# Kernel optimization log

Hardware: AMD Instinct MI355X
Metric: run time of the kernel (lower is better)

## Reference

```python
import jax, jax.numpy as jnp
import numpy as np

N_HEAD = 16
HEAD_DIM = 64  # n_embd // n_head = 1024 // 16


def setup_inputs() -> dict:
    key = jax.random.key(0)
    k1, k2, k3 = jax.random.split(key, 3)
    B, S, D = 2, 2048, 1024
    x = jax.random.normal(k1, (B, S, D), dtype=jnp.float32)
    # torch nn.Linear stores weight [out, in]; we keep [in, out] for x @ W
    w_qkv = jax.random.normal(k2, (D, 3 * D), dtype=jnp.float32) * (D ** -0.5)
    w_proj = jax.random.normal(k3, (D, D), dtype=jnp.float32) * (D ** -0.5)
    return {"x": x, "w_qkv": w_qkv, "w_proj": w_proj}


def reference(x, w_qkv, w_proj):
    B, S, D = x.shape
    qkv = x @ w_qkv  # [B, S, 3D]
    q, k, v = jnp.split(qkv, 3, axis=-1)
    # [B, H, S, hd]
    q = q.reshape(B, S, N_HEAD, HEAD_DIM).transpose(0, 2, 1, 3)
    k = k.reshape(B, S, N_HEAD, HEAD_DIM).transpose(0, 2, 1, 3)
    v = v.reshape(B, S, N_HEAD, HEAD_DIM).transpose(0, 2, 1, 3)
    att = jnp.einsum('bhid,bhjd->bhij', q, k) * (HEAD_DIM ** -0.5)
    causal = jnp.tril(jnp.ones((S, S), dtype=bool))
    att = jnp.where(causal, att, jnp.finfo(att.dtype).min)
    att = jax.nn.softmax(att, axis=-1)
    # dropout p=0 (eval) -> identity
    y = jnp.einsum('bhij,bhjd->bhid', att, v)
    y = y.transpose(0, 2, 1, 3).reshape(B, S, D)
    return y @ w_proj
```

## Files before the change

kernel.cpp:

```cpp
#include <hip/hip_runtime.h>

#define AS1 __attribute__((address_space(1)))
#define AS3 __attribute__((address_space(3)))

using f32x4 = __attribute__((ext_vector_type(4))) float;
using s16x8 = __attribute__((ext_vector_type(8))) short;
using u16x4 = __attribute__((ext_vector_type(4))) unsigned short;
using u32x2 = __attribute__((ext_vector_type(2))) unsigned int;

__device__ __forceinline__ unsigned short f2bf(float f) {
  union { float f; unsigned u; } v; v.f = f;
  unsigned u = v.u;
  return (unsigned short)((u + 0x7FFFu + ((u >> 16) & 1u)) >> 16);
}

__device__ __forceinline__ unsigned pack_bf2(float a, float b) {
  union { float f; unsigned u; } x, y; x.f = a; y.f = b;
  return (x.u >> 16) | (y.u & 0xFFFF0000u);
}

__device__ __forceinline__ void load_lds16(const void* g, void* l) {
  __builtin_amdgcn_global_load_lds((const AS1 void*)g, (AS3 void*)l, 16, 0, 0);
}

__global__ __launch_bounds__(256) void prep_kernel(const float* __restrict__ x,
                                                   const float* __restrict__ w_qkv,
                                                   const float* __restrict__ w_proj,
                                                   unsigned short* __restrict__ xb,
                                                   unsigned short* __restrict__ wqkvT,
                                                   unsigned short* __restrict__ wprojT) {
  __shared__ float tile[32][33];
  const int bid = blockIdx.x, tid = threadIdx.x;
  if (bid < 4096) {
    int i = bid * 256 + tid;
    float4 v = ((const float4*)x)[i];
    u16x4 o;
    o.x = f2bf(v.x); o.y = f2bf(v.y); o.z = f2bf(v.z); o.w = f2bf(v.w);
    ((u16x4*)xb)[i] = o;
    return;
  }
  const float* in;
  unsigned short* out;
  int bx, by, R, C;
  if (bid < 7168) {
    int t = bid - 4096;
    bx = t % 96; by = t / 96; R = 1024; C = 3072;
    in = w_qkv; out = wqkvT;
  } else {
    int t = bid - 7168;
    bx = t % 32; by = t / 32; R = 1024; C = 1024;
    in = w_proj; out = wprojT;
  }
  const int tx = tid & 31, ty = tid >> 5;
  int xcol = bx * 32 + tx;
  int y0 = by * 32;
  for (int j = ty; j < 32; j += 8)
    tile[j][tx] = in[(size_t)(y0 + j) * C + xcol];
  __syncthreads();
  int x2 = by * 32 + tx;
  int y2 = bx * 32;
  for (int j = ty; j < 32; j += 8)
    out[(size_t)(y2 + j) * R + x2] = f2bf(tile[tx][j]);
}

__global__ __launch_bounds__(256) void transpose_v(const unsigned short* __restrict__ qkv,
                                                   unsigned short* __restrict__ Vt) {
  __shared__ unsigned short tile[64][65];
  const int tid = threadIdx.x;
  const int bh = blockIdx.y, b = bh >> 4, h = bh & 15;
  const int s0 = blockIdx.x * 64;
#pragma unroll
  for (int it = 0; it < 2; ++it) {
    int c = tid + it * 256;
    int row = c >> 3, cc = c & 7;
    s16x8 v = *(const s16x8*)(qkv + (size_t)(b * 2048 + s0 + row) * 3072 + 2048 + h * 64 + cc * 8);
#pragma unroll
    for (int j = 0; j < 8; ++j) tile[row][cc * 8 + j] = (unsigned short)v[j];
  }
  __syncthreads();
#pragma unroll
  for (int it = 0; it < 2; ++it) {
    int c = tid + it * 256;
    int d = c >> 3, sc = c & 7;
    s16x8 o;
#pragma unroll
    for (int j = 0; j < 8; ++j) o[j] = (short)tile[sc * 8 + j][d];
    *(s16x8*)(Vt + (size_t)bh * 64 * 2048 + (size_t)d * 2048 + s0 + sc * 8) = o;
  }
}

__global__ __launch_bounds__(256) void gemm_qkv(const unsigned short* __restrict__ A,
                                                const unsigned short* __restrict__ Bt,
                                                unsigned short* __restrict__ C,
                                                int M, int N, int K) {
  __shared__ unsigned short As[128 * 64];
  __shared__ unsigned short Bs[128 * 64];
  const int tid = threadIdx.x;
  const int wave = tid >> 6, lane = tid & 63;
  const int l15 = lane & 15, quad = lane >> 4;
  const int sx = l15 & 7;
  const int wm = wave & 1, wn = wave >> 1;
  const int bm = blockIdx.y, bn = blockIdx.x;

  f32x4 acc[4][4] = {};

  for (int k0 = 0; k0 < K; k0 += 64) {
    __syncthreads();
#pragma unroll
    for (int s = 0; s < 4; ++s) {
      int c = tid + s * 256;
      int row = c >> 3, cc = c & 7;
      int kc = (cc ^ (row & 7)) * 8;
      load_lds16(A + (size_t)(bm * 128 + row) * K + k0 + kc, As + c * 8);
      load_lds16(Bt + (size_t)(bn * 128 + row) * K + k0 + kc, Bs + c * 8);
    }
    __syncthreads();
#pragma unroll
    for (int kk = 0; kk < 2; ++kk) {
      s16x8 af[4], bfr[4];
#pragma unroll
      for (int i = 0; i < 4; ++i) {
        af[i]  = *(const s16x8*)(As + (wm * 64 + i * 16 + l15) * 64 + ((quad + 4 * kk) ^ sx) * 8);
        bfr[i] = *(const s16x8*)(Bs + (wn * 64 + i * 16 + l15) * 64 + ((quad + 4 * kk) ^ sx) * 8);
      }
#pragma unroll
      for (int i = 0; i < 4; ++i)
#pragma unroll
        for (int j = 0; j < 4; ++j)
          acc[i][j] = __builtin_amdgcn_mfma_f32_16x16x32_bf16(af[i], bfr[j], acc[i][j], 0, 0, 0);
    }
  }

  const int row0 = bm * 128 + wm * 64 + quad * 4;
  const int col0 = bn * 128 + wn * 64 + l15;
#pragma unroll
  for (int i = 0; i < 4; ++i)
#pragma unroll
    for (int j = 0; j < 4; ++j)
#pragma unroll
      for (int r = 0; r < 4; ++r)
        C[(size_t)(row0 + i * 16 + r) * N + (col0 + j * 16)] = f2bf(acc[i][j][r]);
}

__global__ __launch_bounds__(256) void gemm_proj(const unsigned short* __restrict__ A,
                                                 const unsigned short* __restrict__ Bt,
                                                 float* __restrict__ C,
                                                 int M, int N, int K) {
  __shared__ unsigned short As[128 * 64];
  __shared__ unsigned short Bs[64 * 64];
  const int tid = threadIdx.x;
  const int wave = tid >> 6, lane = tid & 63;
  const int l15 = lane & 15, quad = lane >> 4;
  const int sx = l15 & 7;
  const int wm = wave & 1, wn = wave >> 1;
  const int bm = blockIdx.y, bn = blockIdx.x;

  f32x4 acc[4][2] = {};

  for (int k0 = 0; k0 < K; k0 += 64) {
    __syncthreads();
#pragma unroll
    for (int s = 0; s < 4; ++s) {
      int c = tid + s * 256;
      int row = c >> 3, cc = c & 7;
      int kc = (cc ^ (row & 7)) * 8;
      load_lds16(A + (size_t)(bm * 128 + row) * K + k0 + kc, As + c * 8);
    }
#pragma unroll
    for (int s = 0; s < 2; ++s) {
      int c = tid + s * 256;
      int row = c >> 3, cc = c & 7;
      int kc = (cc ^ (row & 7)) * 8;
      load_lds16(Bt + (size_t)(bn * 64 + row) * K + k0 + kc, Bs + c * 8);
    }
    __syncthreads();
#pragma unroll
    for (int kk = 0; kk < 2; ++kk) {
      s16x8 af[4], bfr[2];
#pragma unroll
      for (int i = 0; i < 4; ++i)
        af[i] = *(const s16x8*)(As + (wm * 64 + i * 16 + l15) * 64 + ((quad + 4 * kk) ^ sx) * 8);
#pragma unroll
      for (int j = 0; j < 2; ++j)
        bfr[j] = *(const s16x8*)(Bs + (wn * 32 + j * 16 + l15) * 64 + ((quad + 4 * kk) ^ sx) * 8);
#pragma unroll
      for (int i = 0; i < 4; ++i)
#pragma unroll
        for (int j = 0; j < 2; ++j)
          acc[i][j] = __builtin_amdgcn_mfma_f32_16x16x32_bf16(af[i], bfr[j], acc[i][j], 0, 0, 0);
    }
  }

  const int row0 = bm * 128 + wm * 64 + quad * 4;
  const int col0 = bn * 64 + wn * 32 + l15;
#pragma unroll
  for (int i = 0; i < 4; ++i)
#pragma unroll
    for (int j = 0; j < 2; ++j)
#pragma unroll
      for (int r = 0; r < 4; ++r)
        C[(size_t)(row0 + i * 16 + r) * N + (col0 + j * 16)] = acc[i][j][r];
}

__global__ __launch_bounds__(512) void attn_kernel(const unsigned short* __restrict__ qkv,
                                                   const unsigned short* __restrict__ Vt,
                                                   unsigned short* __restrict__ Y) {
  __shared__ unsigned short Qs[128 * 64];
  __shared__ unsigned short Ks[64 * 64];
  __shared__ unsigned short Vs[64 * 64];
  const int tid = threadIdx.x;
  const int wave = tid >> 6, lane = tid & 63;
  const int l15 = lane & 15, quad = lane >> 4;
  const int sx = l15 & 7, sx2 = sx << 1;

  const int p = blockIdx.x;
  const int r_ = p >> 8, c_ = p & 255;
  const int m_ = c_ & 15, g_ = c_ >> 4;
  const int bh = g_ + 16 * r_;
  const int lq = r_ ? (15 - m_) : m_;
  const int q0 = lq * 128;
  const int b = bh >> 4, h = bh & 15;
  const size_t base = (size_t)b * 2048 * 3072 + h * 64;
  const size_t vbase = (size_t)bh * 64 * 2048;

#pragma unroll
  for (int s = 0; s < 2; ++s) {
    int cid = tid + s * 512;
    int row = cid >> 3, cc = cid & 7;
    int kc = (cc ^ (row & 7)) * 8;
    load_lds16(qkv + base + (size_t)(q0 + row) * 3072 + kc, Qs + cid * 8);
  }
  __syncthreads();
  s16x8 qf[2];
  qf[0] = *(const s16x8*)(Qs + (wave * 16 + l15) * 64 + ((quad    ) ^ sx) * 8);
  qf[1] = *(const s16x8*)(Qs + (wave * 16 + l15) * 64 + ((quad + 4) ^ sx) * 8);

  f32x4 o[4] = {};
  float m_i = -1e30f, l_i = 0.f;
  const float kScale = 0.125f * 1.44269504f;
  const int qrow_w0 = q0 + wave * 16;
  const int qrow = qrow_w0 + l15;
  unsigned short* Pw = Qs + wave * 16 * 64;

  for (int j0 = 0; j0 <= q0 + 64; j0 += 64) {
    __syncthreads();
    {
      int row = tid >> 3, cc = tid & 7;
      int kc = (cc ^ (row & 7)) * 8;
      load_lds16(qkv + base + (size_t)(j0 + row) * 3072 + 1024 + kc, Ks + tid * 8);
      load_lds16(Vt + vbase + (size_t)row * 2048 + j0 + kc, Vs + tid * 8);
    }
    __syncthreads();

    if (j0 <= qrow_w0 + 15) {
      f32x4 s[4];
#pragma unroll
      for (int nt = 0; nt < 4; ++nt) {
        const int kr = nt * 16 + l15;
        s16x8 kf0 = *(const s16x8*)(Ks + kr * 64 + ((quad    ) ^ sx) * 8);
        s16x8 kf1 = *(const s16x8*)(Ks + kr * 64 + ((quad + 4) ^ sx) * 8);
        f32x4 z = {};
        z = __builtin_amdgcn_mfma_f32_16x16x32_bf16(kf0, qf[0], z, 0, 0, 0);
        z = __builtin_amdgcn_mfma_f32_16x16x32_bf16(kf1, qf[1], z, 0, 0, 0);
        s[nt] = z;
      }

      if (j0 + 63 > qrow_w0) {
#pragma unroll
        for (int nt = 0; nt < 4; ++nt) {
          int key0 = j0 + nt * 16 + quad * 4;
#pragma unroll
          for (int r = 0; r < 4; ++r)
            if (key0 + r > qrow) s[nt][r] = -3e38f;
        }
      }

      float tmax = s[0][0];
#pragma unroll
      for (int nt = 0; nt < 4; ++nt)
#pragma unroll
        for (int r = 0; r < 4; ++r)
          tmax = fmaxf(tmax, s[nt][r]);
      tmax = fmaxf(tmax, __shfl_xor(tmax, 16, 64));
      tmax = fmaxf(tmax, __shfl_xor(tmax, 32, 64));
      float mn = fmaxf(m_i, tmax);
      float alpha = __builtin_amdgcn_exp2f((m_i - mn) * kScale);
      m_i = mn;
      const float mk = mn * kScale;
      float rsum = 0.f;
#pragma unroll
      for (int nt = 0; nt < 4; ++nt)
#pragma unroll
        for (int r = 0; r < 4; ++r) {
          float pv = __builtin_amdgcn_exp2f(__builtin_fmaf(s[nt][r], kScale, -mk));
          s[nt][r] = pv;
          rsum += pv;
        }
      rsum += __shfl_xor(rsum, 16, 64);
      rsum += __shfl_xor(rsum, 32, 64);
      l_i = l_i * alpha + rsum;
#pragma unroll
      for (int dt = 0; dt < 4; ++dt)
#pragma unroll
        for (int r = 0; r < 4; ++r)
          o[dt][r] *= alpha;

#pragma unroll
      for (int nt = 0; nt < 4; ++nt) {
        u32x2 pk;
        pk.x = pack_bf2(s[nt][0], s[nt][1]);
        pk.y = pack_bf2(s[nt][2], s[nt][3]);
        int phys = (nt * 4 + quad) ^ sx2;
        *(u32x2*)(Pw + l15 * 64 + phys * 4) = pk;
      }

      s16x8 pf[2];
      pf[0] = *(const s16x8*)(Pw + l15 * 64 + (((quad * 2)    ) ^ sx2) * 4);
      pf[1] = *(const s16x8*)(Pw + l15 * 64 + (((quad * 2) + 8) ^ sx2) * 4);

#pragma unroll
      for (int dt = 0; dt < 4; ++dt) {
        const int vr = dt * 16 + l15;
        s16x8 vf0 = *(const s16x8*)(Vs + vr * 64 + ((quad    ) ^ sx) * 8);
        s16x8 vf1 = *(const s16x8*)(Vs + vr * 64 + ((quad + 4) ^ sx) * 8);
        o[dt] = __builtin_amdgcn_mfma_f32_16x16x32_bf16(vf0, pf[0], o[dt], 0, 0, 0);
        o[dt] = __builtin_amdgcn_mfma_f32_16x16x32_bf16(vf1, pf[1], o[dt], 0, 0, 0);
      }
    }
  }

  const float inv = 1.0f / l_i;
  const size_t yoff = (size_t)(b * 2048 + qrow) * 1024 + h * 64 + quad * 4;
#pragma unroll
  for (int dt = 0; dt < 4; ++dt) {
    u16x4 pk;
#pragma unroll
    for (int r = 0; r < 4; ++r) pk[r] = f2bf(o[dt][r] * inv);
    *(u16x4*)(Y + yoff + dt * 16) = pk;
  }
}

extern "C" void kernel_launch(void* const* d_in, const int* in_sizes, int n_in,
                              void* d_out, int out_size, void* d_ws, size_t ws_size,
                              hipStream_t stream) {
  const float* x      = (const float*)d_in[0];
  const float* w_qkv  = (const float*)d_in[1];
  const float* w_proj = (const float*)d_in[2];
  char* ws = (char*)d_ws;
  unsigned short* xb     = (unsigned short*)(ws);
  unsigned short* wqkvT  = (unsigned short*)(ws + (size_t)(8  << 20));
  unsigned short* wprojT = (unsigned short*)(ws + (size_t)(14 << 20));
  unsigned short* qkv    = (unsigned short*)(ws + (size_t)(16 << 20));
  unsigned short* y      = (unsigned short*)(ws + (size_t)(40 << 20));
  unsigned short* Vt     = (unsigned short*)(ws + (size_t)(48 << 20));

  prep_kernel<<<8192, 256, 0, stream>>>(x, w_qkv, w_proj, xb, wqkvT, wprojT);
  gemm_qkv<<<dim3(24, 32), 256, 0, stream>>>(xb, wqkvT, qkv, 4096, 3072, 1024);
  transpose_v<<<dim3(32, 32), 256, 0, stream>>>(qkv, Vt);
  attn_kernel<<<512, 512, 0, stream>>>(qkv, Vt, y);
  gemm_proj<<<dim3(16, 32), 256, 0, stream>>>(y, wprojT, (float*)d_out, 4096, 1024, 1024);
}
```

Measured before the change: 182.9 us.

## Split long causal attention rows across blocks with LUT schedule and combine pass

Attention tiles shrink from 128 to 64 query rows with 256-thread blocks. A constant lookup table gives each of 1536 blocks a query tile and key range. The longer query tiles (t>=16) are split into two key halves whose partial outputs, maxes and sums go to fp32 workspace, and a new combine kernel merges them. The aim is to balance causal work across CUs and shorten the critical path. The cost is an extra kernel launch and partial-result traffic.

New measurement: 188.3 us. 2.9% more time.

```diff
diff --git a/kernel.cpp b/kernel.cpp
--- a/kernel.cpp
+++ b/kernel.cpp
@@ -22,6 +22,16 @@
 __device__ __forceinline__ void load_lds16(const void* g, void* l) {
   __builtin_amdgcn_global_load_lds((const AS1 void*)g, (AS3 void*)l, 16, 0, 0);
 }
+
+__constant__ unsigned char LUT_T[48] = {
+  15,30,31, 8, 7, 0,   31,14,13, 9,16, 1,   28,29,12,10,17, 2,   29,26,24,11,16, 3,
+  30,27,25,22, 6, 4,   27,25,23,20,18, 5,   28,23,21,19,19,17,   26,24,21,22,20,18};
+__constant__ unsigned char LUT_JB[48] = {
+   0, 0, 0, 0, 0, 0,   16, 0, 0, 0, 0, 0,    0, 0, 0, 0, 0, 0,   15, 0, 0, 0, 9, 0,
+  16, 0, 0, 0, 0, 0,   14,13, 0, 0, 0, 0,   15,12, 0, 0,10, 9,   14,13,11,12,11,10};
+__constant__ unsigned char LUT_JE[48] = {
+  16,16,16, 9, 8, 1,   32,15,14,10, 9, 2,   15,15,13,11, 9, 3,   30,14,13,12,17, 4,
+  31,14,13,12, 7, 5,   28,26,12,11,10, 6,   29,24,11,10,20,18,   27,25,22,23,21,19};
 
 __global__ __launch_bounds__(256) void prep_kernel(const float* __restrict__ x,
                                                    const float* __restrict__ w_qkv,
@@ -202,10 +212,13 @@
         C[(size_t)(row0 + i * 16 + r) * N + (col0 + j * 16)] = acc[i][j][r];
 }
 
-__global__ __launch_bounds__(512) void attn_kernel(const unsigned short* __restrict__ qkv,
+__global__ __launch_bounds__(256) void attn_kernel(const unsigned short* __restrict__ qkv,
                                                    const unsigned short* __restrict__ Vt,
-                                                   unsigned short* __restrict__ Y) {
-  __shared__ unsigned short Qs[128 * 64];
+                                                   unsigned short* __restrict__ Y,
+                                                   float* __restrict__ PO,
+                                                   float* __restrict__ PM,
+                                                   float* __restrict__ PL) {
+  __shared__ unsigned short Qs[64 * 64];
   __shared__ unsigned short Ks[64 * 64];
   __shared__ unsigned short Vs[64 * 64];
   const int tid = threadIdx.x;
@@ -214,18 +227,18 @@
   const int sx = l15 & 7, sx2 = sx << 1;
 
   const int p = blockIdx.x;
-  const int r_ = p >> 8, c_ = p & 255;
-  const int m_ = c_ & 15, g_ = c_ >> 4;
-  const int bh = g_ + 16 * r_;
-  const int lq = r_ ? (15 - m_) : m_;
-  const int q0 = lq * 128;
+  const int c_ = p & 255, a_ = p >> 8;
+  const int col = c_ & 7, bh = c_ >> 3;
+  const int li = col * 6 + a_;
+  const int t = LUT_T[li], jbeg = LUT_JB[li], jend = LUT_JE[li];
+  const int q0 = t * 64;
   const int b = bh >> 4, h = bh & 15;
   const size_t base = (size_t)b * 2048 * 3072 + h * 64;
   const size_t vbase = (size_t)bh * 64 * 2048;
 
 #pragma unroll
   for (int s = 0; s < 2; ++s) {
-    int cid = tid + s * 512;
+    int cid = tid + s * 256;
     int row = cid >> 3, cc = cid & 7;
     int kc = (cc ^ (row & 7)) * 8;
     load_lds16(qkv + base + (size_t)(q0 + row) * 3072 + kc, Qs + cid * 8);
@@ -242,101 +255,139 @@
   const int qrow = qrow_w0 + l15;
   unsigned short* Pw = Qs + wave * 16 * 64;
 
-  for (int j0 = 0; j0 <= q0 + 64; j0 += 64) {
-    __syncthreads();
-    {
-      int row = tid >> 3, cc = tid & 7;
+  for (int jt = jbeg; jt < jend; ++jt) {
+    const int j0 = jt * 64;
+    __syncthreads();
+#pragma unroll
+    for (int s = 0; s < 2; ++s) {
+      int c = tid + s * 256;
+      int row = c >> 3, cc = c & 7;
       int kc = (cc ^ (row & 7)) * 8;
-      load_lds16(qkv + base + (size_t)(j0 + row) * 3072 + 1024 + kc, Ks + tid * 8);
-      load_lds16(Vt + vbase + (size_t)row * 2048 + j0 + kc, Vs + tid * 8);
-    }
-    __syncthreads();
-
-    if (j0 <= qrow_w0 + 15) {
-      f32x4 s[4];
+      load_lds16(qkv + base + (size_t)(j0 + row) * 3072 + 1024 + kc, Ks + c * 8);
+      load_lds16(Vt + vbase + (size_t)row * 2048 + j0 + kc, Vs + c * 8);
+    }
+    __syncthreads();
+
+    f32x4 s[4];
+#pragma unroll
+    for (int nt = 0; nt < 4; ++nt) {
+      const int kr = nt * 16 + l15;
+      s16x8 kf0 = *(const s16x8*)(Ks + kr * 64 + ((quad    ) ^ sx) * 8);
+      s16x8 kf1 = *(const s16x8*)(Ks + kr * 64 + ((quad + 4) ^ sx) * 8);
+      f32x4 z = {};
+      z = __builtin_amdgcn_mfma_f32_16x16x32_bf16(kf0, qf[0], z, 0, 0, 0);
+      z = __builtin_amdgcn_mfma_f32_16x16x32_bf16(kf1, qf[1], z, 0, 0, 0);
+      s[nt] = z;
+    }
+
+    if (j0 + 63 > qrow_w0) {
 #pragma unroll
       for (int nt = 0; nt < 4; ++nt) {
-        const int kr = nt * 16 + l15;
-        s16x8 kf0 = *(const s16x8*)(Ks + kr * 64 + ((quad    ) ^ sx) * 8);
-        s16x8 kf1 = *(const s16x8*)(Ks + kr * 64 + ((quad + 4) ^ sx) * 8);
-        f32x4 z = {};
-        z = __builtin_amdgcn_mfma_f32_16x16x32_bf16(kf0, qf[0], z, 0, 0, 0);
-        z = __builtin_amdgcn_mfma_f32_16x16x32_bf16(kf1, qf[1], z, 0, 0, 0);
-        s[nt] = z;
+        int key0 = j0 + nt * 16 + quad * 4;
+#pragma unroll
+        for (int r = 0; r < 4; ++r)
+          if (key0 + r > qrow) s[nt][r] = -3e38f;
       }
-
-      if (j0 + 63 > qrow_w0) {
-#pragma unroll
-        for (int nt = 0; nt < 4; ++nt) {
-          int key0 = j0 + nt * 16 + quad * 4;
-#pragma unroll
-          for (int r = 0; r < 4; ++r)
-            if (key0 + r > qrow) s[nt][r] = -3e38f;
-        }
+    }
+
+    float tmax = s[0][0];
+#pragma unroll
+    for (int nt = 0; nt < 4; ++nt)
+#pragma unroll
+      for (int r = 0; r < 4; ++r)
+        tmax = fmaxf(tmax, s[nt][r]);
+    tmax = fmaxf(tmax, __shfl_xor(tmax, 16, 64));
+    tmax = fmaxf(tmax, __shfl_xor(tmax, 32, 64));
+    float mn = fmaxf(m_i, tmax);
+    float alpha = __builtin_amdgcn_exp2f((m_i - mn) * kScale);
+    m_i = mn;
+    const float mk = mn * kScale;
+    float rsum = 0.f;
+#pragma unroll
+    for (int nt = 0; nt < 4; ++nt)
+#pragma unroll
+      for (int r = 0; r < 4; ++r) {
+        float pv = __builtin_amdgcn_exp2f(__builtin_fmaf(s[nt][r], kScale, -mk));
+        s[nt][r] = pv;
+        rsum += pv;
       }
-
-      float tmax = s[0][0];
-#pragma unroll
-      for (int nt = 0; nt < 4; ++nt)
-#pragma unroll
-        for (int r = 0; r < 4; ++r)
-          tmax = fmaxf(tmax, s[nt][r]);
-      tmax = fmaxf(tmax, __shfl_xor(tmax, 16, 64));
-      tmax = fmaxf(tmax, __shfl_xor(tmax, 32, 64));
-      float mn = fmaxf(m_i, tmax);
-      float alpha = __builtin_amdgcn_exp2f((m_i - mn) * kScale);
-      m_i = mn;
-      const float mk = mn * kScale;
-      float rsum = 0.f;
-#pragma unroll
-      for (int nt = 0; nt < 4; ++nt)
-#pragma unroll
-        for (int r = 0; r < 4; ++r) {
-          float pv = __builtin_amdgcn_exp2f(__builtin_fmaf(s[nt][r], kScale, -mk));
-          s[nt][r] = pv;
-          rsum += pv;
-        }
-      rsum += __shfl_xor(rsum, 16, 64);
-      rsum += __shfl_xor(rsum, 32, 64);
-      l_i = l_i * alpha + rsum;
-#pragma unroll
-      for (int dt = 0; dt < 4; ++dt)
-#pragma unroll
-        for (int r = 0; r < 4; ++r)
-          o[dt][r] *= alpha;
-
-#pragma unroll
-      for (int nt = 0; nt < 4; ++nt) {
-        u32x2 pk;
-        pk.x = pack_bf2(s[nt][0], s[nt][1]);
-        pk.y = pack_bf2(s[nt][2], s[nt][3]);
-        int phys = (nt * 4 + quad) ^ sx2;
-        *(u32x2*)(Pw + l15 * 64 + phys * 4) = pk;
-      }
-
-      s16x8 pf[2];
-      pf[0] = *(const s16x8*)(Pw + l15 * 64 + (((quad * 2)    ) ^ sx2) * 4);
-      pf[1] = *(const s16x8*)(Pw + l15 * 64 + (((quad * 2) + 8) ^ sx2) * 4);
-
-#pragma unroll
-      for (int dt = 0; dt < 4; ++dt) {
-        const int vr = dt * 16 + l15;
-        s16x8 vf0 = *(const s16x8*)(Vs + vr * 64 + ((quad    ) ^ sx) * 8);
-        s16x8 vf1 = *(const s16x8*)(Vs + vr * 64 + ((quad + 4) ^ sx) * 8);
-        o[dt] = __builtin_amdgcn_mfma_f32_16x16x32_bf16(vf0, pf[0], o[dt], 0, 0, 0);
-        o[dt] = __builtin_amdgcn_mfma_f32_16x16x32_bf16(vf1, pf[1], o[dt], 0, 0, 0);
-      }
-    }
-  }
-
-  const float inv = 1.0f / l_i;
-  const size_t yoff = (size_t)(b * 2048 + qrow) * 1024 + h * 64 + quad * 4;
-#pragma unroll
-  for (int dt = 0; dt < 4; ++dt) {
-    u16x4 pk;
-#pragma unroll
-    for (int r = 0; r < 4; ++r) pk[r] = f2bf(o[dt][r] * inv);
-    *(u16x4*)(Y + yoff + dt * 16) = pk;
+    rsum += __shfl_xor(rsum, 16, 64);
+    rsum += __shfl_xor(rsum, 32, 64);
+    l_i = l_i * alpha + rsum;
+#pragma unroll
+    for (int dt = 0; dt < 4; ++dt)
+#pragma unroll
+      for (int r = 0; r < 4; ++r)
+        o[dt][r] *= alpha;
+
+#pragma unroll
+    for (int nt = 0; nt < 4; ++nt) {
+      u32x2 pk;
+      pk.x = pack_bf2(s[nt][0], s[nt][1]);
+      pk.y = pack_bf2(s[nt][2], s[nt][3]);
+      int phys = (nt * 4 + quad) ^ sx2;
+      *(u32x2*)(Pw + l15 * 64 + phys * 4) = pk;
+    }
+
+    s16x8 pf[2];
+    pf[0] = *(const s16x8*)(Pw + l15 * 64 + (((quad * 2)    ) ^ sx2) * 4);
+    pf[1] = *(const s16x8*)(Pw + l15 * 64 + (((quad * 2) + 8) ^ sx2) * 4);
+
+#pragma unroll
+    for (int dt = 0; dt < 4; ++dt) {
+      const int vr = dt * 16 + l15;
+      s16x8 vf0 = *(const s16x8*)(Vs + vr * 64 + ((quad    ) ^ sx) * 8);
+      s16x8 vf1 = *(const s16x8*)(Vs + vr * 64 + ((quad + 4) ^ sx) * 8);
+      o[dt] = __builtin_amdgcn_mfma_f32_16x16x32_bf16(vf0, pf[0], o[dt], 0, 0, 0);
+      o[dt] = __builtin_amdgcn_mfma_f32_16x16x32_bf16(vf1, pf[1], o[dt], 0, 0, 0);
+    }
+  }
+
+  if (t < 16) {
+    const float inv = 1.0f / l_i;
+    const size_t yoff = (size_t)(b * 2048 + qrow) * 1024 + h * 64 + quad * 4;
+#pragma unroll
+    for (int dt = 0; dt < 4; ++dt) {
+      u16x4 pk;
+#pragma unroll
+      for (int r = 0; r < 4; ++r) pk[r] = f2bf(o[dt][r] * inv);
+      *(u16x4*)(Y + yoff + dt * 16) = pk;
+    }
+  } else {
+    const int half = (jbeg == 0) ? 0 : 1;
+    const int idx = (bh * 16 + (t - 16)) * 2 + half;
+    const int qlocal = wave * 16 + l15;
+    float* POb = PO + (size_t)idx * 4096 + qlocal * 64;
+#pragma unroll
+    for (int dt = 0; dt < 4; ++dt)
+      *(f32x4*)(POb + dt * 16 + quad * 4) = o[dt];
+    if (quad == 0) {
+      PM[idx * 64 + qlocal] = m_i;
+      PL[idx * 64 + qlocal] = l_i;
+    }
+  }
+}
+
+__global__ __launch_bounds__(256) void attn_combine(const float* __restrict__ PO,
+                                                    const float* __restrict__ PM,
+                                                    const float* __restrict__ PL,
+                                                    unsigned short* __restrict__ Y) {
+  const int tid = threadIdx.x;
+  const int d = tid & 63;
+  const float kScale = 0.125f * 1.44269504f;
+  for (int it = 0; it < 16; ++it) {
+    int R = blockIdx.x * 64 + it * 4 + (tid >> 6);
+    int bh = R >> 10, rem = R & 1023, tp = rem >> 6, q = rem & 63;
+    int i2 = (bh * 16 + tp) * 2;
+    float m1 = PM[i2 * 64 + q], l1 = PL[i2 * 64 + q];
+    float m2 = PM[(i2 + 1) * 64 + q], l2 = PL[(i2 + 1) * 64 + q];
+    float m = fmaxf(m1, m2);
+    float a1 = __builtin_amdgcn_exp2f((m1 - m) * kScale);
+    float a2 = __builtin_amdgcn_exp2f((m2 - m) * kScale);
+    size_t o1 = (size_t)i2 * 4096 + q * 64 + d;
+    float v = (PO[o1] * a1 + PO[o1 + 4096] * a2) / (l1 * a1 + l2 * a2);
+    int b = bh >> 4, h = bh & 15, qrow = (tp + 16) * 64 + q;
+    Y[(size_t)(b * 2048 + qrow) * 1024 + h * 64 + d] = f2bf(v);
   }
 }
 
@@ -353,10 +404,14 @@
   unsigned short* qkv    = (unsigned short*)(ws + (size_t)(16 << 20));
   unsigned short* y      = (unsigned short*)(ws + (size_t)(40 << 20));
   unsigned short* Vt     = (unsigned short*)(ws + (size_t)(48 << 20));
+  float*          PO     = (float*)(ws + (size_t)(56 << 20));
+  float*          PM     = (float*)(ws + (size_t)(73 << 20));
+  float*          PL     = (float*)(ws + (size_t)(74 << 20));
 
   prep_kernel<<<8192, 256, 0, stream>>>(x, w_qkv, w_proj, xb, wqkvT, wprojT);
   gemm_qkv<<<dim3(24, 32), 256, 0, stream>>>(xb, wqkvT, qkv, 4096, 3072, 1024);
   transpose_v<<<dim3(32, 32), 256, 0, stream>>>(qkv, Vt);
-  attn_kernel<<<512, 512, 0, stream>>>(qkv, Vt, y);
+  attn_kernel<<<1536, 256, 0, stream>>>(qkv, Vt, y, PO, PM, PL);
+  attn_combine<<<512, 256, 0, stream>>>(PO, PM, PL, y);
   gemm_proj<<<dim3(16, 32), 256, 0, stream>>>(y, wprojT, (float*)d_out, 4096, 1024, 1024);
 }
```

## Compute V transposed directly via GEMM and double-buffer K/V tiles in attention

Applied to the files above, without the earlier changes.

Splits the QKV projection into a Q/K GEMM and a separate GEMM that writes V already transposed (W_v^T · x^T), so the standalone V transpose kernel is no longer needed. The attention kernel now reads from the narrower QK buffer and the new Vt layout. It also double-buffers the K/V shared-memory tiles, prefetching the next tile while the current one is computed, with one barrier per iteration instead of two. This costs more LDS per block, and the Vt GEMM uses a smaller M tile.

Measured after the change: 186.0 us. No clear change (+1.7%).

```diff
diff --git a/kernel.cpp b/kernel.cpp
--- a/kernel.cpp
+++ b/kernel.cpp
@@ -63,36 +63,10 @@
     out[(size_t)(y2 + j) * R + x2] = f2bf(tile[tx][j]);
 }
 
-__global__ __launch_bounds__(256) void transpose_v(const unsigned short* __restrict__ qkv,
-                                                   unsigned short* __restrict__ Vt) {
-  __shared__ unsigned short tile[64][65];
-  const int tid = threadIdx.x;
-  const int bh = blockIdx.y, b = bh >> 4, h = bh & 15;
-  const int s0 = blockIdx.x * 64;
-#pragma unroll
-  for (int it = 0; it < 2; ++it) {
-    int c = tid + it * 256;
-    int row = c >> 3, cc = c & 7;
-    s16x8 v = *(const s16x8*)(qkv + (size_t)(b * 2048 + s0 + row) * 3072 + 2048 + h * 64 + cc * 8);
-#pragma unroll
-    for (int j = 0; j < 8; ++j) tile[row][cc * 8 + j] = (unsigned short)v[j];
-  }
-  __syncthreads();
-#pragma unroll
-  for (int it = 0; it < 2; ++it) {
-    int c = tid + it * 256;
-    int d = c >> 3, sc = c & 7;
-    s16x8 o;
-#pragma unroll
-    for (int j = 0; j < 8; ++j) o[j] = (short)tile[sc * 8 + j][d];
-    *(s16x8*)(Vt + (size_t)bh * 64 * 2048 + (size_t)d * 2048 + s0 + sc * 8) = o;
-  }
-}
-
-__global__ __launch_bounds__(256) void gemm_qkv(const unsigned short* __restrict__ A,
-                                                const unsigned short* __restrict__ Bt,
-                                                unsigned short* __restrict__ C,
-                                                int M, int N, int K) {
+__global__ __launch_bounds__(256) void gemm_qk(const unsigned short* __restrict__ A,
+                                               const unsigned short* __restrict__ Bt,
+                                               unsigned short* __restrict__ C,
+                                               int M, int N, int K) {
   __shared__ unsigned short As[128 * 64];
   __shared__ unsigned short Bs[128 * 64];
   const int tid = threadIdx.x;
@@ -135,6 +109,70 @@
   const int col0 = bn * 128 + wn * 64 + l15;
 #pragma unroll
   for (int i = 0; i < 4; ++i)
+#pragma unroll
+    for (int j = 0; j < 4; ++j)
+#pragma unroll
+      for (int r = 0; r < 4; ++r)
+        C[(size_t)(row0 + i * 16 + r) * N + (col0 + j * 16)] = f2bf(acc[i][j][r]);
+}
+
+__global__ __launch_bounds__(256) void gemm_vt(const unsigned short* __restrict__ A,
+                                               const unsigned short* __restrict__ Bt,
+                                               unsigned short* __restrict__ C,
+                                               int M, int N, int K) {
+  __shared__ unsigned short As[64 * 64];
+  __shared__ unsigned short Bs[128 * 64];
+  const int tid = threadIdx.x;
+  const int wave = tid >> 6, lane = tid & 63;
+  const int l15 = lane & 15, quad = lane >> 4;
+  const int sx = l15 & 7;
+  const int wm = wave & 1, wn = wave >> 1;
+  const int bm = blockIdx.y, bn = blockIdx.x;
+
+  f32x4 acc[2][4] = {};
+
+  for (int k0 = 0; k0 < K; k0 += 64) {
+    __syncthreads();
+    {
+      int c = tid;
+#pragma unroll
+      for (int s = 0; s < 2; ++s, c += 256) {
+        int row = c >> 3, cc = c & 7;
+        int kc = (cc ^ (row & 7)) * 8;
+        load_lds16(A + (size_t)(bm * 64 + row) * K + k0 + kc, As + c * 8);
+      }
+    }
+    {
+      int c = tid;
+#pragma unroll
+      for (int s = 0; s < 4; ++s, c += 256) {
+        int row = c >> 3, cc = c & 7;
+        int kc = (cc ^ (row & 7)) * 8;
+        load_lds16(Bt + (size_t)(bn * 128 + row) * K + k0 + kc, Bs + c * 8);
+      }
+    }
+    __syncthreads();
+#pragma unroll
+    for (int kk = 0; kk < 2; ++kk) {
+      s16x8 af[2], bfr[4];
+#pragma unroll
+      for (int i = 0; i < 2; ++i)
+        af[i] = *(const s16x8*)(As + (wm * 32 + i * 16 + l15) * 64 + ((quad + 4 * kk) ^ sx) * 8);
+#pragma unroll
+      for (int j = 0; j < 4; ++j)
+        bfr[j] = *(const s16x8*)(Bs + (wn * 64 + j * 16 + l15) * 64 + ((quad + 4 * kk) ^ sx) * 8);
+#pragma unroll
+      for (int i = 0; i < 2; ++i)
+#pragma unroll
+        for (int j = 0; j < 4; ++j)
+          acc[i][j] = __builtin_amdgcn_mfma_f32_16x16x32_bf16(af[i], bfr[j], acc[i][j], 0, 0, 0);
+    }
+  }
+
+  const int row0 = bm * 64 + wm * 32 + quad * 4;
+  const int col0 = bn * 128 + wn * 64 + l15;
+#pragma unroll
+  for (int i = 0; i < 2; ++i)
 #pragma unroll
     for (int j = 0; j < 4; ++j)
 #pragma unroll
@@ -202,12 +240,12 @@
         C[(size_t)(row0 + i * 16 + r) * N + (col0 + j * 16)] = acc[i][j][r];
 }
 
-__global__ __launch_bounds__(512) void attn_kernel(const unsigned short* __restrict__ qkv,
+__global__ __launch_bounds__(512) void attn_kernel(const unsigned short* __restrict__ qk,
                                                    const unsigned short* __restrict__ Vt,
                                                    unsigned short* __restrict__ Y) {
   __shared__ unsigned short Qs[128 * 64];
-  __shared__ unsigned short Ks[64 * 64];
-  __shared__ unsigned short Vs[64 * 64];
+  __shared__ unsigned short Ks[2][64 * 64];
+  __shared__ unsigned short Vs[2][64 * 64];
   const int tid = threadIdx.x;
   const int wave = tid >> 6, lane = tid & 63;
   const int l15 = lane & 15, quad = lane >> 4;
@@ -220,17 +258,23 @@
   const int lq = r_ ? (15 - m_) : m_;
   const int q0 = lq * 128;
   const int b = bh >> 4, h = bh & 15;
-  const size_t base = (size_t)b * 2048 * 3072 + h * 64;
-  const size_t vbase = (size_t)bh * 64 * 2048;
+  const size_t base = (size_t)b * 2048 * 2048 + h * 64;
+  const size_t vtb = (size_t)(h * 64) * 4096 + b * 2048;
+
+  const int srow = tid >> 3, scc = tid & 7;
+  const int skc = (scc ^ (srow & 7)) * 8;
 
 #pragma unroll
   for (int s = 0; s < 2; ++s) {
     int cid = tid + s * 512;
     int row = cid >> 3, cc = cid & 7;
     int kc = (cc ^ (row & 7)) * 8;
-    load_lds16(qkv + base + (size_t)(q0 + row) * 3072 + kc, Qs + cid * 8);
-  }
+    load_lds16(qk + base + (size_t)(q0 + row) * 2048 + kc, Qs + cid * 8);
+  }
+  load_lds16(qk + base + (size_t)srow * 2048 + 1024 + skc, &Ks[0][0] + tid * 8);
+  load_lds16(Vt + vtb + (size_t)srow * 4096 + skc, &Vs[0][0] + tid * 8);
   __syncthreads();
+
   s16x8 qf[2];
   qf[0] = *(const s16x8*)(Qs + (wave * 16 + l15) * 64 + ((quad    ) ^ sx) * 8);
   qf[1] = *(const s16x8*)(Qs + (wave * 16 + l15) * 64 + ((quad + 4) ^ sx) * 8);
@@ -242,23 +286,26 @@
   const int qrow = qrow_w0 + l15;
   unsigned short* Pw = Qs + wave * 16 * 64;
 
-  for (int j0 = 0; j0 <= q0 + 64; j0 += 64) {
-    __syncthreads();
-    {
-      int row = tid >> 3, cc = tid & 7;
-      int kc = (cc ^ (row & 7)) * 8;
-      load_lds16(qkv + base + (size_t)(j0 + row) * 3072 + 1024 + kc, Ks + tid * 8);
-      load_lds16(Vt + vbase + (size_t)row * 2048 + j0 + kc, Vs + tid * 8);
-    }
-    __syncthreads();
+  const int nIters = (q0 >> 6) + 2;
+  for (int jt = 0; jt < nIters; ++jt) {
+    const int j0 = jt << 6;
+    const int cur = jt & 1;
+    if (jt + 1 < nIters) {
+      const int jn = j0 + 64, nxt = cur ^ 1;
+      load_lds16(qk + base + (size_t)(jn + srow) * 2048 + 1024 + skc, &Ks[nxt][0] + tid * 8);
+      load_lds16(Vt + vtb + (size_t)srow * 4096 + jn + skc, &Vs[nxt][0] + tid * 8);
+    }
 
     if (j0 <= qrow_w0 + 15) {
+      const unsigned short* Ksb = &Ks[cur][0];
+      const unsigned short* Vsb = &Vs[cur][0];
+
       f32x4 s[4];
 #pragma unroll
       for (int nt = 0; nt < 4; ++nt) {
         const int kr = nt * 16 + l15;
-        s16x8 kf0 = *(const s16x8*)(Ks + kr * 64 + ((quad    ) ^ sx) * 8);
-        s16x8 kf1 = *(const s16x8*)(Ks + kr * 64 + ((quad + 4) ^ sx) * 8);
+        s16x8 kf0 = *(const s16x8*)(Ksb + kr * 64 + ((quad    ) ^ sx) * 8);
+        s16x8 kf1 = *(const s16x8*)(Ksb + kr * 64 + ((quad + 4) ^ sx) * 8);
         f32x4 z = {};
         z = __builtin_amdgcn_mfma_f32_16x16x32_bf16(kf0, qf[0], z, 0, 0, 0);
         z = __builtin_amdgcn_mfma_f32_16x16x32_bf16(kf1, qf[1], z, 0, 0, 0);
@@ -321,12 +368,13 @@
 #pragma unroll
       for (int dt = 0; dt < 4; ++dt) {
         const int vr = dt * 16 + l15;
-        s16x8 vf0 = *(const s16x8*)(Vs + vr * 64 + ((quad    ) ^ sx) * 8);
-        s16x8 vf1 = *(const s16x8*)(Vs + vr * 64 + ((quad + 4) ^ sx) * 8);
+        s16x8 vf0 = *(const s16x8*)(Vsb + vr * 64 + ((quad    ) ^ sx) * 8);
+        s16x8 vf1 = *(const s16x8*)(Vsb + vr * 64 + ((quad + 4) ^ sx) * 8);
         o[dt] = __builtin_amdgcn_mfma_f32_16x16x32_bf16(vf0, pf[0], o[dt], 0, 0, 0);
         o[dt] = __builtin_amdgcn_mfma_f32_16x16x32_bf16(vf1, pf[1], o[dt], 0, 0, 0);
       }
     }
+    __syncthreads();
   }
 
   const float inv = 1.0f / l_i;
@@ -350,13 +398,13 @@
   unsigned short* xb     = (unsigned short*)(ws);
   unsigned short* wqkvT  = (unsigned short*)(ws + (size_t)(8  << 20));
   unsigned short* wprojT = (unsigned short*)(ws + (size_t)(14 << 20));
-  unsigned short* qkv    = (unsigned short*)(ws + (size_t)(16 << 20));
+  unsigned short* qk     = (unsigned short*)(ws + (size_t)(16 << 20));
   unsigned short* y      = (unsigned short*)(ws + (size_t)(40 << 20));
   unsigned short* Vt     = (unsigned short*)(ws + (size_t)(48 << 20));
 
   prep_kernel<<<8192, 256, 0, stream>>>(x, w_qkv, w_proj, xb, wqkvT, wprojT);
-  gemm_qkv<<<dim3(24, 32), 256, 0, stream>>>(xb, wqkvT, qkv, 4096, 3072, 1024);
-  transpose_v<<<dim3(32, 32), 256, 0, stream>>>(qkv, Vt);
-  attn_kernel<<<512, 512, 0, stream>>>(qkv, Vt, y);
+  gemm_qk<<<dim3(16, 32), 256, 0, stream>>>(xb, wqkvT, qk, 4096, 2048, 1024);
+  gemm_vt<<<dim3(32, 16), 256, 0, stream>>>(wqkvT + (size_t)2048 * 1024, xb, Vt, 1024, 4096, 1024);
+  attn_kernel<<<512, 512, 0, stream>>>(qk, Vt, y);
   gemm_proj<<<dim3(16, 32), 256, 0, stream>>>(y, wprojT, (float*)d_out, 4096, 1024, 1024);
 }
```
